# Optimization experiments

Measured on AMD Instinct MI355X. Metric: run time of the kernel, lower is better.

Reference implementation:

```python
import jax, jax.numpy as jnp
import numpy as np

B, N, L, E, U, G, R, D, C = 64, 50000, 8, 100000, 20000, 20000, 64, 16, 2


def setup_inputs() -> dict:
    rng = np.random.default_rng(0)
    key = jax.random.key(0)
    ks = jax.random.split(key, 10)
    # index structures (duplicate-free where the torch code assumes uniqueness)
    gene_map = jnp.asarray(rng.choice(N, G, replace=False).astype(np.int32))
    dst_unique = jnp.stack([jnp.asarray(rng.choice(N, U, replace=False).astype(np.int32)) for _ in range(L)])
    root_ids = jnp.asarray(rng.choice(N, R, replace=False).astype(np.int32))
    src = jax.random.randint(ks[0], (L, E), 0, N, dtype=jnp.int32)
    dst_pos = jax.random.randint(ks[1], (L, E), 0, U, dtype=jnp.int32)
    # data and parameters
    X_gene_batch = jax.random.normal(ks[2], (B, G), jnp.float32)
    w_in = jax.random.normal(ks[3], (D,), jnp.float32) * 0.5   # Linear(1, d) weight
    b_in = jax.random.normal(ks[4], (D,), jnp.float32) * 0.1
    W = jax.random.normal(ks[5], (L, D, D), jnp.float32) * (1.0 / np.sqrt(D))  # xavier-ish
    bias = jnp.zeros((N, D), jnp.float32)
    W_head = jax.random.normal(ks[6], (C, R * D), jnp.float32) * (1.0 / np.sqrt(R * D))
    b_head = jnp.zeros((C,), jnp.float32)
    return {
        "X_gene_batch": X_gene_batch, "w_in": w_in, "b_in": b_in, "W": W,
        "bias": bias, "W_head": W_head, "b_head": b_head,
        "gene_map": gene_map, "src": src, "dst_pos": dst_pos,
        "dst_unique": dst_unique, "root_ids": root_ids,
    }


def reference(X_gene_batch, w_in, b_in, W, bias, W_head, b_head,
              gene_map, src, dst_pos, dst_unique, root_ids):
    Bn = X_gene_batch.shape[0]
    n_nodes, d = bias.shape
    n_layers = W.shape[0]
    u = dst_unique.shape[1]
    # _init_state_vector: h=0, scatter in_proj(X[...,None]) at gene_map
    gene_emb = X_gene_batch[..., None] * w_in + b_in          # [B, G, d]
    h = jnp.zeros((Bn, n_nodes, d), X_gene_batch.dtype)
    h = h.at[:, gene_map].set(gene_emb)
    for li in range(n_layers):
        h_src = h[:, src[li]]                                  # gather [B, E, d]
        msg = jnp.einsum('bed,df->bef', h_src, W[li])          # small dxd matmul
        agg = jnp.zeros((Bn, u, d), h.dtype).at[:, dst_pos[li]].add(msg)  # scatter-add
        h_dst = jnp.tanh(agg + bias[dst_unique[li]][None])     # bias lookup + tanh (dropout=0)
        h = h.at[:, dst_unique[li]].set(h_dst)                 # write back
    feat = h[:, root_ids].reshape(Bn, -1)                      # roots_concat readout
    return feat @ W_head.T + b_head                            # [B, C]
```

## Files before the change

### kernel.cpp

```cpp
#include <hip/hip_runtime.h>
#include <hip/hip_fp16.h>
#include <cmath>

constexpr int B_ = 64, N_ = 50000, L_ = 8, E_ = 100000, U_ = 20000, G_ = 20000, R_ = 64, D_ = 16, C_ = 2;
constexpr int EPL_ = E_ + 3 * U_ + 4096;
constexpr int EPLG_ = EPL_ / 4 + 16;
constexpr int GPW = 8;
constexpr int BC = 64;
constexpr int F = BC * 2;


__device__ __forceinline__ float tanh_fast(float x) {
  float e = __expf(2.0f * x);
  return 1.0f - 2.0f * __builtin_amdgcn_rcpf(e + 1.0f);
}


__global__ __launch_bounds__(256) void hist_kernel(
    const int* __restrict__ dst_pos, int* __restrict__ cnt,
    int* __restrict__ rank) {
  int e = blockIdx.x * 256 + threadIdx.x;
  int li = blockIdx.y;
  if (e >= E_) return;
  rank[li * E_ + e] = atomicAdd(&cnt[li * U_ + dst_pos[li * E_ + e]], 1);
}

__global__ __launch_bounds__(1024) void scan_kernel(
    const int* __restrict__ cnt, int* __restrict__ offs) {
  __shared__ int sums[1024];
  int li = blockIdx.x, t = threadIdx.x;
  int base = t * 20;
  int v[20];
  int s = 0;
#pragma unroll
  for (int i = 0; i < 20; ++i) {
    int idx = base + i;
    int c = (idx < U_) ? cnt[li * U_ + idx] : -1;
    int pc = (c < 0) ? 0 : ((c == 0) ? 4 : ((c + 3) & ~3));
    v[i] = s;
    s += pc;
  }
  sums[t] = s;
  __syncthreads();
  for (int off = 1; off < 1024; off <<= 1) {
    int o = (t >= off) ? sums[t - off] : 0;
    __syncthreads();
    sums[t] += o;
    __syncthreads();
  }
  int excl = sums[t] - s;
#pragma unroll
  for (int i = 0; i < 20; ++i) {
    int idx = base + i;
    if (idx < U_) offs[li * (U_ + 1) + idx] = excl + v[i];
  }
  if (t == 1023) offs[li * (U_ + 1) + U_] = sums[1023];
}

__global__ __launch_bounds__(256) void scatter_kernel(
    const int* __restrict__ dst_pos, const int* __restrict__ src,
    const int* __restrict__ offs, const int* __restrict__ rank,
    int* __restrict__ ssrc) {
  int e = blockIdx.x * 256 + threadIdx.x;
  int li = blockIdx.y;
  if (e >= E_) return;
  int u = dst_pos[li * E_ + e];
  int p = offs[li * (U_ + 1) + u] + rank[li * E_ + e];
  ssrc[(size_t)li * EPL_ + p] = src[li * E_ + e];
}

__global__ __launch_bounds__(256) void pad_fill_ug_k(
    const int* __restrict__ cnt, const int* __restrict__ offs,
    int* __restrict__ ssrc, int* __restrict__ ug) {
  int t = blockIdx.x * 256 + threadIdx.x;
  if (t >= L_ * U_) return;
  int li = t / U_, u = t % U_;
  int start = offs[li * (U_ + 1) + u];
  int end = start + cnt[li * U_ + u];
  int pend = offs[li * (U_ + 1) + u + 1];
  int* sp = ssrc + (size_t)li * EPL_;
  for (int p = end; p < pend; ++p) sp[p] = N_;
  int* ugp = ug + (size_t)li * EPLG_;
  for (int g = start >> 2; g < (pend >> 2); ++g) ugp[g] = u;
  if (u == U_ - 1) {
    int ptot = offs[li * (U_ + 1) + U_];
    for (int p = ptot; p < ptot + 8; ++p) sp[p] = N_;
  }
}


__global__ __launch_bounds__(256) void gene_init_k(
    const float* __restrict__ X, const float* __restrict__ w_in,
    const float* __restrict__ b_in, const int* __restrict__ gene_map,
    float4* __restrict__ h4) {
  int t = blockIdx.x * 256 + threadIdx.x;
  if (t >= G_ * BC) return;
  int b = t % BC;
  int g = t / BC;
  float x = X[b * G_ + g];
  int node = gene_map[g];
  float4 out[2];
  __half2* oh = reinterpret_cast<__half2*>(out);
#pragma unroll
  for (int k = 0; k < 8; ++k) {
    float r0 = fmaf(x, w_in[2 * k], b_in[2 * k]);
    float r1 = fmaf(x, w_in[2 * k + 1], b_in[2 * k + 1]);
    oh[k] = __float22half2_rn(make_float2(r0, r1));
  }
  h4[(size_t)node * F + b * 2] = out[0];
  h4[(size_t)node * F + b * 2 + 1] = out[1];
}

__global__ __launch_bounds__(256) void gather_k(
    const float4* __restrict__ h4, const int* __restrict__ ug,
    const int* __restrict__ ssrc, float4* __restrict__ agg4, int li) {
  int tid = threadIdx.x;
  int wave = tid >> 6, lane = tid & 63;
  int wv = blockIdx.x * 4 + wave;
  int g0 = wv * GPW, gend = g0 + GPW;
  const int* ugp = ug + (size_t)li * EPLG_;
  const int* sp = ssrc + (size_t)li * EPL_;

  int prevU = (g0 == 0) ? -2 : ugp[g0 - 1];
  int g = g0;
  while (g < gend && ugp[g] == prevU) ++g;
  if (g >= gend) return;
  int curU = ugp[g];
  if (curU < 0) return;

  __half2 acc[2][2][4];
  const __half2 z = __half2half2(__float2half(0.f));
#pragma unroll
  for (int j = 0; j < 2; ++j)
#pragma unroll
    for (int r = 0; r < 2; ++r)
#pragma unroll
      for (int k = 0; k < 4; ++k) acc[j][r][k] = z;

  auto flushu = [&](int u) {
#pragma unroll
    for (int r = 0; r < 2; ++r) {
      float4 outv;
      __half2* ov = reinterpret_cast<__half2*>(&outv);
#pragma unroll
      for (int k = 0; k < 4; ++k) {
        float2 f0 = __half22float2(acc[0][r][k]);
        float2 f1 = __half22float2(acc[1][r][k]);
        ov[k] = __float22half2_rn(make_float2(f0.x + f1.x, f0.y + f1.y));
      }
      agg4[(size_t)u * F + lane + r * 64] = outv;
    }
#pragma unroll
    for (int j = 0; j < 2; ++j)
#pragma unroll
      for (int r = 0; r < 2; ++r)
#pragma unroll
        for (int k = 0; k < 4; ++k) acc[j][r][k] = z;
  };

  auto loadRows = [&](float4 (&v)[4][2], int4 id) {
    v[0][0] = h4[(size_t)id.x * F + lane]; v[0][1] = h4[(size_t)id.x * F + lane + 64];
    v[1][0] = h4[(size_t)id.y * F + lane]; v[1][1] = h4[(size_t)id.y * F + lane + 64];
    v[2][0] = h4[(size_t)id.z * F + lane]; v[2][1] = h4[(size_t)id.z * F + lane + 64];
    v[3][0] = h4[(size_t)id.w * F + lane]; v[3][1] = h4[(size_t)id.w * F + lane + 64];
  };
  auto accum = [&](const float4 (&v)[4][2]) {
#pragma unroll
    for (int j = 0; j < 4; ++j)
#pragma unroll
      for (int r = 0; r < 2; ++r) {
        const __half2* p = reinterpret_cast<const __half2*>(&v[j][r]);
#pragma unroll
        for (int k = 0; k < 4; ++k)
          acc[j & 1][r][k] = __hadd2(acc[j & 1][r][k], p[k]);
      }
  };

  float4 va[4][2], vb[4][2];
  int4 idA = *(const int4*)(sp + 4 * g);
  loadRows(va, idA);
  int nuA = ugp[g + 1];
  int nuB;

  for (;;) {
    {
      bool more = (nuA >= 0) && ((nuA == curU) || (g + 1 < gend));
      if (more) {
        int4 idB = *(const int4*)(sp + 4 * (g + 1));
        loadRows(vb, idB);
        nuB = ugp[g + 2];
      }
      accum(va);
      if (nuA != curU) {
        flushu(curU);
        if (!more) return;
        curU = nuA;
      }
      ++g;
    }
    {
      bool more = (nuB >= 0) && ((nuB == curU) || (g + 1 < gend));
      if (more) {
        int4 idA2 = *(const int4*)(sp + 4 * (g + 1));
        loadRows(va, idA2);
        nuA = ugp[g + 2];
      }
      accum(vb);
      if (nuB != curU) {
        flushu(curU);
        if (!more) return;
        curU = nuB;
      }
      ++g;
    }
  }
}

__global__ __launch_bounds__(256) void dense_k(
    const float4* __restrict__ agg4, const float* __restrict__ W,
    const float* __restrict__ bias, const int* __restrict__ dst_unique,
    float4* __restrict__ h4, int li) {
  __shared__ float Wlds[256];
  int tid = threadIdx.x;
  Wlds[tid] = W[li * 256 + tid];
  __syncthreads();
  int t = blockIdx.x * 256 + tid;
  int u = t >> 6, b = t & 63;
  float4 c0 = agg4[(size_t)u * F + b * 2];
  float4 c1 = agg4[(size_t)u * F + b * 2 + 1];
  float a[16];
  {
    const __half2* p0 = reinterpret_cast<const __half2*>(&c0);
    const __half2* p1 = reinterpret_cast<const __half2*>(&c1);
#pragma unroll
    for (int k = 0; k < 4; ++k) {
      float2 f0 = __half22float2(p0[k]);
      float2 f1 = __half22float2(p1[k]);
      a[2 * k] = f0.x; a[2 * k + 1] = f0.y;
      a[8 + 2 * k] = f1.x; a[8 + 2 * k + 1] = f1.y;
    }
  }
  float m[16];
#pragma unroll
  for (int j = 0; j < 16; ++j) m[j] = 0.f;
#pragma unroll
  for (int d = 0; d < 16; ++d) {
    float s = a[d];
    const float4* wr = (const float4*)&Wlds[d * 16];
    float4 w0 = wr[0], w1 = wr[1], w2 = wr[2], w3 = wr[3];
    m[0] = fmaf(s, w0.x, m[0]);  m[1] = fmaf(s, w0.y, m[1]);
    m[2] = fmaf(s, w0.z, m[2]);  m[3] = fmaf(s, w0.w, m[3]);
    m[4] = fmaf(s, w1.x, m[4]);  m[5] = fmaf(s, w1.y, m[5]);
    m[6] = fmaf(s, w1.z, m[6]);  m[7] = fmaf(s, w1.w, m[7]);
    m[8] = fmaf(s, w2.x, m[8]);  m[9] = fmaf(s, w2.y, m[9]);
    m[10] = fmaf(s, w2.z, m[10]); m[11] = fmaf(s, w2.w, m[11]);
    m[12] = fmaf(s, w3.x, m[12]); m[13] = fmaf(s, w3.y, m[13]);
    m[14] = fmaf(s, w3.z, m[14]); m[15] = fmaf(s, w3.w, m[15]);
  }
  int node = dst_unique[li * U_ + u];
  const float4* bp = (const float4*)(bias + (size_t)node * 16);
  float4 b0 = bp[0], b1 = bp[1], b2 = bp[2], b3 = bp[3];
  float bb[16] = {b0.x, b0.y, b0.z, b0.w, b1.x, b1.y, b1.z, b1.w,
                  b2.x, b2.y, b2.z, b2.w, b3.x, b3.y, b3.z, b3.w};
  float4 o0, o1;
  __half2* ov0 = reinterpret_cast<__half2*>(&o0);
  __half2* ov1 = reinterpret_cast<__half2*>(&o1);
#pragma unroll
  for (int k = 0; k < 4; ++k) {
    ov0[k] = __float22half2_rn(make_float2(tanh_fast(m[2 * k] + bb[2 * k]),
                                           tanh_fast(m[2 * k + 1] + bb[2 * k + 1])));
    ov1[k] = __float22half2_rn(make_float2(tanh_fast(m[8 + 2 * k] + bb[8 + 2 * k]),
                                           tanh_fast(m[8 + 2 * k + 1] + bb[8 + 2 * k + 1])));
  }
  h4[(size_t)node * F + b * 2] = o0;
  h4[(size_t)node * F + b * 2 + 1] = o1;
}

__global__ __launch_bounds__(64) void head_k(
    const float4* __restrict__ h4, const float* __restrict__ W_head,
    const float* __restrict__ b_head, const int* __restrict__ root_ids,
    float* __restrict__ out) {
  int bl = blockIdx.x;
  int r = threadIdx.x;
  int node = root_ids[r];
  float4 p0 = h4[(size_t)node * F + bl * 2];
  float4 p1 = h4[(size_t)node * F + bl * 2 + 1];
  float v[16];
  const __half2* ph0 = reinterpret_cast<const __half2*>(&p0);
  const __half2* ph1 = reinterpret_cast<const __half2*>(&p1);
#pragma unroll
  for (int k = 0; k < 4; ++k) {
    float2 f0 = __half22float2(ph0[k]);
    float2 f1 = __half22float2(ph1[k]);
    v[2 * k] = f0.x; v[2 * k + 1] = f0.y;
    v[8 + 2 * k] = f1.x; v[8 + 2 * k + 1] = f1.y;
  }
  float acc0 = 0.f, acc1 = 0.f;
#pragma unroll
  for (int d = 0; d < 16; ++d) {
    acc0 = fmaf(v[d], W_head[r * 16 + d], acc0);
    acc1 = fmaf(v[d], W_head[1024 + r * 16 + d], acc1);
  }
  for (int off = 32; off; off >>= 1) {
    acc0 += __shfl_down(acc0, off, 64);
    acc1 += __shfl_down(acc1, off, 64);
  }
  if (r == 0) {
    out[bl * 2 + 0] = acc0 + b_head[0];
    out[bl * 2 + 1] = acc1 + b_head[1];
  }
}

__global__ void zero_out_k(float* out, int n) {
  int t = blockIdx.x * 256 + threadIdx.x;
  if (t < n) out[t] = 0.f;
}


static size_t need_bytes() {
  return (size_t)(N_ + 1) * F * 16 + (size_t)U_ * F * 16 +
         (size_t)L_ * U_ * 4 +
         (size_t)L_ * (U_ + 1) * 4 +
         (size_t)L_ * E_ * 4 +
         (size_t)L_ * EPL_ * 4;
}

extern "C" void kernel_launch(void* const* d_in, const int* in_sizes, int n_in,
                              void* d_out, int out_size, void* d_ws, size_t ws_size,
                              hipStream_t stream) {
  if (ws_size < need_bytes()) {
    zero_out_k<<<(out_size + 255) / 256, 256, 0, stream>>>((float*)d_out, out_size);
    return;
  }
  const float* X = (const float*)d_in[0];
  const float* w_in = (const float*)d_in[1];
  const float* b_in = (const float*)d_in[2];
  const float* W = (const float*)d_in[3];
  const float* bias = (const float*)d_in[4];
  const float* W_head = (const float*)d_in[5];
  const float* b_head = (const float*)d_in[6];
  const int* gene_map = (const int*)d_in[7];
  const int* src = (const int*)d_in[8];
  const int* dst_pos = (const int*)d_in[9];
  const int* dst_unique = (const int*)d_in[10];
  const int* root_ids = (const int*)d_in[11];
  float* out = (float*)d_out;

  const size_t h_bytes = (size_t)(N_ + 1) * F * 16;
  const size_t agg_bytes = (size_t)U_ * F * 16;
  const size_t cnt_bytes = (size_t)L_ * U_ * 4;
  const size_t offs_bytes = (size_t)L_ * (U_ + 1) * 4;
  const size_t rank_bytes = (size_t)L_ * E_ * 4;
  const size_t ug_bytes = (size_t)L_ * EPLG_ * 4;

  char* ws = (char*)d_ws;
  float4* h4 = (float4*)ws;
  float4* agg4 = (float4*)(ws + h_bytes);
  int* cnt = (int*)(ws + h_bytes + agg_bytes);
  int* offs = (int*)(ws + h_bytes + agg_bytes + cnt_bytes);
  int* rank = (int*)(ws + h_bytes + agg_bytes + cnt_bytes + offs_bytes);
  int* ug = rank;
  int* ssrc = (int*)(ws + h_bytes + agg_bytes + cnt_bytes + offs_bytes + rank_bytes);
  (void)ug_bytes;

  hipMemsetAsync(cnt, 0, cnt_bytes, stream);
  hipMemsetAsync(h4, 0, h_bytes, stream);
  dim3 egrid((E_ + 255) / 256, L_);
  hist_kernel<<<egrid, 256, 0, stream>>>(dst_pos, cnt, rank);
  scan_kernel<<<L_, 1024, 0, stream>>>(cnt, offs);
  scatter_kernel<<<egrid, 256, 0, stream>>>(dst_pos, src, offs, rank, ssrc);
  hipMemsetAsync(ug, 0xFF, ug_bytes, stream);
  pad_fill_ug_k<<<(L_ * U_ + 255) / 256, 256, 0, stream>>>(cnt, offs, ssrc, ug);

  gene_init_k<<<(G_ * BC + 255) / 256, 256, 0, stream>>>(X, w_in, b_in, gene_map, h4);

  const int total_groups = EPL_ / 4;
  const int gwaves = (total_groups + GPW - 1) / GPW;
  const int gather_grid = (gwaves + 3) / 4;
  const int dense_grid = U_ * BC / 256;
  for (int li = 0; li < L_; ++li) {
    gather_k<<<gather_grid, 256, 0, stream>>>(h4, ug, ssrc, agg4, li);
    dense_k<<<dense_grid, 256, 0, stream>>>(agg4, W, bias, dst_unique, h4, li);
  }

  head_k<<<BC, 64, 0, stream>>>(h4, W_head, b_head, root_ids, out);
}
```

Measured before the change: 631.2 us.

## Split gather rows across two waves, deepen prefetch, and fuse padding into scan

The gather kernel now assigns each group span to two waves, each handling one half of the 128-float4 row. It adds an 8-deep ring of index prefetches with 4 outstanding row-load batches, which raises memory-level parallelism per wave while lowering register use per wave. The padding and ug-fill work moves into the scan kernel, which removes one kernel launch and one memset. ug gets its own workspace region instead of aliasing rank, which is needed because rank is still being read while the scatter kernel runs. The cost is a larger workspace, duplicated index loads across the two waves, and serial per-thread fill loops inside the single-block-per-layer scan.

```diff
diff --git a/kernel.cpp b/kernel.cpp
--- a/kernel.cpp
+++ b/kernel.cpp
@@ -25,17 +25,20 @@
   rank[li * E_ + e] = atomicAdd(&cnt[li * U_ + dst_pos[li * E_ + e]], 1);
 }
 
-__global__ __launch_bounds__(1024) void scan_kernel(
-    const int* __restrict__ cnt, int* __restrict__ offs) {
+__global__ __launch_bounds__(1024) void scan_pad_kernel(
+    const int* __restrict__ cnt, int* __restrict__ offs,
+    int* __restrict__ ssrc, int* __restrict__ ug) {
   __shared__ int sums[1024];
   int li = blockIdx.x, t = threadIdx.x;
   int base = t * 20;
+  int cr[20];
   int v[20];
   int s = 0;
 #pragma unroll
   for (int i = 0; i < 20; ++i) {
     int idx = base + i;
     int c = (idx < U_) ? cnt[li * U_ + idx] : -1;
+    cr[i] = c;
     int pc = (c < 0) ? 0 : ((c == 0) ? 4 : ((c + 3) & ~3));
     v[i] = s;
     s += pc;
@@ -49,12 +52,24 @@
     __syncthreads();
   }
   int excl = sums[t] - s;
+  int* sp = ssrc + (size_t)li * EPL_;
+  int* ugp = ug + (size_t)li * EPLG_;
 #pragma unroll
   for (int i = 0; i < 20; ++i) {
     int idx = base + i;
-    if (idx < U_) offs[li * (U_ + 1) + idx] = excl + v[i];
-  }
-  if (t == 1023) offs[li * (U_ + 1) + U_] = sums[1023];
+    if (idx >= U_) break;
+    int start = excl + v[i];
+    int c = cr[i];
+    int pc = (c == 0) ? 4 : ((c + 3) & ~3);
+    int pend = start + pc;
+    offs[li * (U_ + 1) + idx] = start;
+    for (int p = start + c; p < pend; ++p) sp[p] = N_;
+    for (int gq = start >> 2; gq < (pend >> 2); ++gq) ugp[gq] = idx;
+  }
+  int ptot = sums[1023];
+  if (t == 1023) offs[li * (U_ + 1) + U_] = ptot;
+  for (int p = ptot + t; p < EPL_; p += 1024) sp[p] = N_;
+  for (int gq = (ptot >> 2) + t; gq < EPLG_; gq += 1024) ugp[gq] = -1;
 }
 
 __global__ __launch_bounds__(256) void scatter_kernel(
@@ -67,25 +82,6 @@
   int u = dst_pos[li * E_ + e];
   int p = offs[li * (U_ + 1) + u] + rank[li * E_ + e];
   ssrc[(size_t)li * EPL_ + p] = src[li * E_ + e];
-}
-
-__global__ __launch_bounds__(256) void pad_fill_ug_k(
-    const int* __restrict__ cnt, const int* __restrict__ offs,
-    int* __restrict__ ssrc, int* __restrict__ ug) {
-  int t = blockIdx.x * 256 + threadIdx.x;
-  if (t >= L_ * U_) return;
-  int li = t / U_, u = t % U_;
-  int start = offs[li * (U_ + 1) + u];
-  int end = start + cnt[li * U_ + u];
-  int pend = offs[li * (U_ + 1) + u + 1];
-  int* sp = ssrc + (size_t)li * EPL_;
-  for (int p = end; p < pend; ++p) sp[p] = N_;
-  int* ugp = ug + (size_t)li * EPLG_;
-  for (int g = start >> 2; g < (pend >> 2); ++g) ugp[g] = u;
-  if (u == U_ - 1) {
-    int ptot = offs[li * (U_ + 1) + U_];
-    for (int p = ptot; p < ptot + 8; ++p) sp[p] = N_;
-  }
 }
 
 
@@ -114,12 +110,16 @@
 __global__ __launch_bounds__(256) void gather_k(
     const float4* __restrict__ h4, const int* __restrict__ ug,
     const int* __restrict__ ssrc, float4* __restrict__ agg4, int li) {
+  constexpr int GCAP = EPL_ / 4;
   int tid = threadIdx.x;
-  int wave = tid >> 6, lane = tid & 63;
-  int wv = blockIdx.x * 4 + wave;
-  int g0 = wv * GPW, gend = g0 + GPW;
+  int lane = tid & 63;
+  int wv = __builtin_amdgcn_readfirstlane(blockIdx.x * 4 + (tid >> 6));
+  int span = wv >> 1, half = wv & 1;
+  int g0 = span * GPW, gend = g0 + GPW;
   const int* ugp = ug + (size_t)li * EPLG_;
   const int* sp = ssrc + (size_t)li * EPL_;
+  const float4* hb = h4 + ((half << 6) + lane);
+  float4* ab = agg4 + ((half << 6) + lane);
 
   int prevU = (g0 == 0) ? -2 : ugp[g0 - 1];
   int g = g0;
@@ -128,92 +128,103 @@
   int curU = ugp[g];
   if (curU < 0) return;
 
-  __half2 acc[2][2][4];
+  __half2 acc0[4], acc1[4];
   const __half2 z = __half2half2(__float2half(0.f));
 #pragma unroll
-  for (int j = 0; j < 2; ++j)
-#pragma unroll
-    for (int r = 0; r < 2; ++r)
-#pragma unroll
-      for (int k = 0; k < 4; ++k) acc[j][r][k] = z;
-
-  auto flushu = [&](int u) {
-#pragma unroll
-    for (int r = 0; r < 2; ++r) {
-      float4 outv;
-      __half2* ov = reinterpret_cast<__half2*>(&outv);
-#pragma unroll
-      for (int k = 0; k < 4; ++k) {
-        float2 f0 = __half22float2(acc[0][r][k]);
-        float2 f1 = __half22float2(acc[1][r][k]);
-        ov[k] = __float22half2_rn(make_float2(f0.x + f1.x, f0.y + f1.y));
-      }
-      agg4[(size_t)u * F + lane + r * 64] = outv;
+  for (int k = 0; k < 4; ++k) { acc0[k] = z; acc1[k] = z; }
+
+  auto FLUSH = [&](int u) {
+    float4 outv;
+    __half2* ov = reinterpret_cast<__half2*>(&outv);
+#pragma unroll
+    for (int k = 0; k < 4; ++k) {
+      float2 f0 = __half22float2(acc0[k]);
+      float2 f1 = __half22float2(acc1[k]);
+      ov[k] = __float22half2_rn(make_float2(f0.x + f1.x, f0.y + f1.y));
+      acc0[k] = z;
+      acc1[k] = z;
     }
-#pragma unroll
-    for (int j = 0; j < 2; ++j)
-#pragma unroll
-      for (int r = 0; r < 2; ++r)
-#pragma unroll
-        for (int k = 0; k < 4; ++k) acc[j][r][k] = z;
+    ab[(size_t)u << 7] = outv;
   };
 
-  auto loadRows = [&](float4 (&v)[4][2], int4 id) {
-    v[0][0] = h4[(size_t)id.x * F + lane]; v[0][1] = h4[(size_t)id.x * F + lane + 64];
-    v[1][0] = h4[(size_t)id.y * F + lane]; v[1][1] = h4[(size_t)id.y * F + lane + 64];
-    v[2][0] = h4[(size_t)id.z * F + lane]; v[2][1] = h4[(size_t)id.z * F + lane + 64];
-    v[3][0] = h4[(size_t)id.w * F + lane]; v[3][1] = h4[(size_t)id.w * F + lane + 64];
+  auto LDROWS = [&](float4 (&vv)[4], const int4& id) {
+    vv[0] = hb[(size_t)id.x << 7];
+    vv[1] = hb[(size_t)id.y << 7];
+    vv[2] = hb[(size_t)id.z << 7];
+    vv[3] = hb[(size_t)id.w << 7];
   };
-  auto accum = [&](const float4 (&v)[4][2]) {
-#pragma unroll
-    for (int j = 0; j < 4; ++j)
-#pragma unroll
-      for (int r = 0; r < 2; ++r) {
-        const __half2* p = reinterpret_cast<const __half2*>(&v[j][r]);
-#pragma unroll
-        for (int k = 0; k < 4; ++k)
-          acc[j & 1][r][k] = __hadd2(acc[j & 1][r][k], p[k]);
-      }
+
+  auto ACCUM = [&](const float4 (&vv)[4]) {
+    const __half2* q0 = reinterpret_cast<const __half2*>(&vv[0]);
+    const __half2* q1 = reinterpret_cast<const __half2*>(&vv[1]);
+    const __half2* q2 = reinterpret_cast<const __half2*>(&vv[2]);
+    const __half2* q3 = reinterpret_cast<const __half2*>(&vv[3]);
+#pragma unroll
+    for (int k = 0; k < 4; ++k) {
+      acc0[k] = __hadd2(acc0[k], q0[k]);
+      acc1[k] = __hadd2(acc1[k], q1[k]);
+      acc0[k] = __hadd2(acc0[k], q2[k]);
+      acc1[k] = __hadd2(acc1[k], q3[k]);
+    }
   };
 
-  float4 va[4][2], vb[4][2];
-  int4 idA = *(const int4*)(sp + 4 * g);
-  loadRows(va, idA);
-  int nuA = ugp[g + 1];
-  int nuB;
+  int gstart = g;
+  int gA = gstart & ~7;
+  int4 idq0, idq1, idq2, idq3, idq4, idq5, idq6, idq7;
+  int nu0, nu1, nu2, nu3, nu4, nu5, nu6, nu7;
+
+#define QINIT(K)                                     \
+  {                                                  \
+    int gq_ = gA + K;                                \
+    if (gq_ < gstart) {                              \
+      idq##K = make_int4(N_, N_, N_, N_);            \
+      nu##K = curU;                                  \
+    } else {                                         \
+      gq_ = (gq_ < GCAP) ? gq_ : GCAP - 1;           \
+      idq##K = *(const int4*)(sp + 4 * gq_);         \
+      nu##K = ugp[gq_ + 1];                          \
+    }                                                \
+  }
+  QINIT(0) QINIT(1) QINIT(2) QINIT(3) QINIT(4) QINIT(5) QINIT(6) QINIT(7)
+
+  float4 v0[4], v1[4], v2[4], v3[4];
+  LDROWS(v0, idq0);
+  LDROWS(v1, idq1);
+  LDROWS(v2, idq2);
+  LDROWS(v3, idq3);
+  g = gA;
+
+#define PHASE(K, VB, IDU)                            \
+  {                                                  \
+    ACCUM(VB);                                       \
+    int nu_ = nu##K;                                 \
+    if (nu_ != curU) {                               \
+      FLUSH(curU);                                   \
+      if (nu_ < 0 || g + 1 >= gend) return;          \
+      curU = nu_;                                    \
+    }                                                \
+    ++g;                                             \
+    {                                                \
+      int gq_ = g + 7;                               \
+      gq_ = (gq_ < GCAP) ? gq_ : GCAP - 1;           \
+      idq##K = *(const int4*)(sp + 4 * gq_);         \
+      nu##K = ugp[gq_ + 1];                          \
+    }                                                \
+    LDROWS(VB, idq##IDU);                            \
+  }
 
   for (;;) {
-    {
-      bool more = (nuA >= 0) && ((nuA == curU) || (g + 1 < gend));
-      if (more) {
-        int4 idB = *(const int4*)(sp + 4 * (g + 1));
-        loadRows(vb, idB);
-        nuB = ugp[g + 2];
-      }
-      accum(va);
-      if (nuA != curU) {
-        flushu(curU);
-        if (!more) return;
-        curU = nuA;
-      }
-      ++g;
-    }
-    {
-      bool more = (nuB >= 0) && ((nuB == curU) || (g + 1 < gend));
-      if (more) {
-        int4 idA2 = *(const int4*)(sp + 4 * (g + 1));
-        loadRows(va, idA2);
-        nuA = ugp[g + 2];
-      }
-      accum(vb);
-      if (nuB != curU) {
-        flushu(curU);
-        if (!more) return;
-        curU = nuB;
-      }
-      ++g;
-    }
-  }
+    PHASE(0, v0, 4)
+    PHASE(1, v1, 5)
+    PHASE(2, v2, 6)
+    PHASE(3, v3, 7)
+    PHASE(4, v0, 0)
+    PHASE(5, v1, 1)
+    PHASE(6, v2, 2)
+    PHASE(7, v3, 3)
+  }
+#undef PHASE
+#undef QINIT
 }
 
 __global__ __launch_bounds__(256) void dense_k(
@@ -224,8 +235,8 @@
   int tid = threadIdx.x;
   Wlds[tid] = W[li * 256 + tid];
   __syncthreads();
-  int t = blockIdx.x * 256 + tid;
-  int u = t >> 6, b = t & 63;
+  int u = __builtin_amdgcn_readfirstlane(blockIdx.x * 4 + (tid >> 6));
+  int b = tid & 63;
   float4 c0 = agg4[(size_t)u * F + b * 2];
   float4 c1 = agg4[(size_t)u * F + b * 2 + 1];
   float a[16];
@@ -322,7 +333,8 @@
          (size_t)L_ * U_ * 4 +
          (size_t)L_ * (U_ + 1) * 4 +
          (size_t)L_ * E_ * 4 +
-         (size_t)L_ * EPL_ * 4;
+         (size_t)L_ * EPL_ * 4 +
+         (size_t)L_ * EPLG_ * 4;
 }
 
 extern "C" void kernel_launch(void* const* d_in, const int* in_sizes, int n_in,
@@ -351,7 +363,7 @@
   const size_t cnt_bytes = (size_t)L_ * U_ * 4;
   const size_t offs_bytes = (size_t)L_ * (U_ + 1) * 4;
   const size_t rank_bytes = (size_t)L_ * E_ * 4;
-  const size_t ug_bytes = (size_t)L_ * EPLG_ * 4;
+  const size_t ssrc_bytes = (size_t)L_ * EPL_ * 4;
 
   char* ws = (char*)d_ws;
   float4* h4 = (float4*)ws;
@@ -359,24 +371,22 @@
   int* cnt = (int*)(ws + h_bytes + agg_bytes);
   int* offs = (int*)(ws + h_bytes + agg_bytes + cnt_bytes);
   int* rank = (int*)(ws + h_bytes + agg_bytes + cnt_bytes + offs_bytes);
-  int* ug = rank;
   int* ssrc = (int*)(ws + h_bytes + agg_bytes + cnt_bytes + offs_bytes + rank_bytes);
-  (void)ug_bytes;
+  int* ug = (int*)(ws + h_bytes + agg_bytes + cnt_bytes + offs_bytes + rank_bytes + ssrc_bytes);
 
   hipMemsetAsync(cnt, 0, cnt_bytes, stream);
   hipMemsetAsync(h4, 0, h_bytes, stream);
   dim3 egrid((E_ + 255) / 256, L_);
   hist_kernel<<<egrid, 256, 0, stream>>>(dst_pos, cnt, rank);
-  scan_kernel<<<L_, 1024, 0, stream>>>(cnt, offs);
+  scan_pad_kernel<<<L_, 1024, 0, stream>>>(cnt, offs, ssrc, ug);
   scatter_kernel<<<egrid, 256, 0, stream>>>(dst_pos, src, offs, rank, ssrc);
-  hipMemsetAsync(ug, 0xFF, ug_bytes, stream);
-  pad_fill_ug_k<<<(L_ * U_ + 255) / 256, 256, 0, stream>>>(cnt, offs, ssrc, ug);
 
   gene_init_k<<<(G_ * BC + 255) / 256, 256, 0, stream>>>(X, w_in, b_in, gene_map, h4);
 
   const int total_groups = EPL_ / 4;
   const int gwaves = (total_groups + GPW - 1) / GPW;
-  const int gather_grid = (gwaves + 3) / 4;
+  const int gather_waves = gwaves * 2;
+  const int gather_grid = (gather_waves + 3) / 4;
   const int dense_grid = U_ * BC / 256;
   for (int li = 0; li < L_; ++li) {
     gather_k<<<gather_grid, 256, 0, stream>>>(h4, ug, ssrc, agg4, li);
```

After: 716.7 us. 13.5% more time.

## Fuse padding into scan and deepen gather prefetch to three stages

Applied to the files above, without the earlier changes.

Merges the pad-fill and ug-labeling pass into the scan kernel, which removes one kernel launch and one memset. ug gets its own workspace region instead of aliasing rank. The gather kernel moves from a 2-deep to a 3-deep software pipeline of row loads, computes its stop group up front, and uses readfirstlane to keep wave indices scalar. This hides more gather latency at the cost of extra registers, and the scan kernel now does serial padding writes per thread.

```diff
diff --git a/kernel.cpp b/kernel.cpp
--- a/kernel.cpp
+++ b/kernel.cpp
@@ -25,17 +25,20 @@
   rank[li * E_ + e] = atomicAdd(&cnt[li * U_ + dst_pos[li * E_ + e]], 1);
 }
 
-__global__ __launch_bounds__(1024) void scan_kernel(
-    const int* __restrict__ cnt, int* __restrict__ offs) {
+__global__ __launch_bounds__(1024) void scan_pad_kernel(
+    const int* __restrict__ cnt, int* __restrict__ offs,
+    int* __restrict__ ssrc, int* __restrict__ ug) {
   __shared__ int sums[1024];
   int li = blockIdx.x, t = threadIdx.x;
   int base = t * 20;
+  int cr[20];
   int v[20];
   int s = 0;
 #pragma unroll
   for (int i = 0; i < 20; ++i) {
     int idx = base + i;
     int c = (idx < U_) ? cnt[li * U_ + idx] : -1;
+    cr[i] = c;
     int pc = (c < 0) ? 0 : ((c == 0) ? 4 : ((c + 3) & ~3));
     v[i] = s;
     s += pc;
@@ -49,12 +52,24 @@
     __syncthreads();
   }
   int excl = sums[t] - s;
+  int* sp = ssrc + (size_t)li * EPL_;
+  int* ugp = ug + (size_t)li * EPLG_;
 #pragma unroll
   for (int i = 0; i < 20; ++i) {
     int idx = base + i;
-    if (idx < U_) offs[li * (U_ + 1) + idx] = excl + v[i];
-  }
-  if (t == 1023) offs[li * (U_ + 1) + U_] = sums[1023];
+    if (idx >= U_) break;
+    int start = excl + v[i];
+    int c = cr[i];
+    int pc = (c == 0) ? 4 : ((c + 3) & ~3);
+    int pend = start + pc;
+    offs[li * (U_ + 1) + idx] = start;
+    for (int p = start + c; p < pend; ++p) sp[p] = N_;
+    for (int gq = start >> 2; gq < (pend >> 2); ++gq) ugp[gq] = idx;
+  }
+  int ptot = sums[1023];
+  if (t == 1023) offs[li * (U_ + 1) + U_] = ptot;
+  for (int p = ptot + t; p < EPL_; p += 1024) sp[p] = N_;
+  for (int gq = (ptot >> 2) + t; gq < EPLG_; gq += 1024) ugp[gq] = -1;
 }
 
 __global__ __launch_bounds__(256) void scatter_kernel(
@@ -67,25 +82,6 @@
   int u = dst_pos[li * E_ + e];
   int p = offs[li * (U_ + 1) + u] + rank[li * E_ + e];
   ssrc[(size_t)li * EPL_ + p] = src[li * E_ + e];
-}
-
-__global__ __launch_bounds__(256) void pad_fill_ug_k(
-    const int* __restrict__ cnt, const int* __restrict__ offs,
-    int* __restrict__ ssrc, int* __restrict__ ug) {
-  int t = blockIdx.x * 256 + threadIdx.x;
-  if (t >= L_ * U_) return;
-  int li = t / U_, u = t % U_;
-  int start = offs[li * (U_ + 1) + u];
-  int end = start + cnt[li * U_ + u];
-  int pend = offs[li * (U_ + 1) + u + 1];
-  int* sp = ssrc + (size_t)li * EPL_;
-  for (int p = end; p < pend; ++p) sp[p] = N_;
-  int* ugp = ug + (size_t)li * EPLG_;
-  for (int g = start >> 2; g < (pend >> 2); ++g) ugp[g] = u;
-  if (u == U_ - 1) {
-    int ptot = offs[li * (U_ + 1) + U_];
-    for (int p = ptot; p < ptot + 8; ++p) sp[p] = N_;
-  }
 }
 
 
@@ -114,9 +110,10 @@
 __global__ __launch_bounds__(256) void gather_k(
     const float4* __restrict__ h4, const int* __restrict__ ug,
     const int* __restrict__ ssrc, float4* __restrict__ agg4, int li) {
+  constexpr int GCAP = EPL_ / 4;
   int tid = threadIdx.x;
-  int wave = tid >> 6, lane = tid & 63;
-  int wv = blockIdx.x * 4 + wave;
+  int lane = tid & 63;
+  int wv = __builtin_amdgcn_readfirstlane(blockIdx.x * 4 + (tid >> 6));
   int g0 = wv * GPW, gend = g0 + GPW;
   const int* ugp = ug + (size_t)li * EPLG_;
   const int* sp = ssrc + (size_t)li * EPL_;
@@ -127,6 +124,16 @@
   if (g >= gend) return;
   int curU = ugp[g];
   if (curU < 0) return;
+
+  int uend = ugp[gend - 1];
+  int gstop;
+  if (uend < 0) {
+    gstop = g;
+    while (ugp[gstop] >= 0) ++gstop;
+  } else {
+    gstop = gend;
+    while (ugp[gstop] == uend) ++gstop;
+  }
 
   __half2 acc[2][2][4];
   const __half2 z = __half2half2(__float2half(0.f));
@@ -176,44 +183,42 @@
       }
   };
 
-  float4 va[4][2], vb[4][2];
-  int4 idA = *(const int4*)(sp + 4 * g);
-  loadRows(va, idA);
+  auto CLG = [&](int q) { return (q < GCAP) ? q : GCAP - 1; };
+
+  int4 id0 = *(const int4*)(sp + 4 * g);
+  int4 id1 = *(const int4*)(sp + 4 * CLG(g + 1));
+  int4 idP = *(const int4*)(sp + 4 * CLG(g + 2));
+  int4 idQ = *(const int4*)(sp + 4 * CLG(g + 3));
+  int4 idR;
   int nuA = ugp[g + 1];
-  int nuB;
+  int nuB = ugp[CLG(g + 1) + 1];
+  int nuC = ugp[CLG(g + 2) + 1];
+
+  float4 va[4][2], vb[4][2], vc[4][2];
+  loadRows(va, id0);
+  loadRows(vb, id1);
+
+#define PHASE(VACC, VLD, IDLD, IDPF, NUCUR)          \
+  {                                                  \
+    loadRows(VLD, IDLD);                             \
+    IDPF = *(const int4*)(sp + 4 * CLG(g + 4));      \
+    int nuCur = NUCUR;                               \
+    NUCUR = ugp[CLG(g + 3) + 1];                     \
+    accum(VACC);                                     \
+    if (nuCur != curU) {                             \
+      flushu(curU);                                  \
+      if (g + 1 >= gstop) return;                    \
+      curU = nuCur;                                  \
+    }                                                \
+    ++g;                                             \
+  }
 
   for (;;) {
-    {
-      bool more = (nuA >= 0) && ((nuA == curU) || (g + 1 < gend));
-      if (more) {
-        int4 idB = *(const int4*)(sp + 4 * (g + 1));
-        loadRows(vb, idB);
-        nuB = ugp[g + 2];
-      }
-      accum(va);
-      if (nuA != curU) {
-        flushu(curU);
-        if (!more) return;
-        curU = nuA;
-      }
-      ++g;
-    }
-    {
-      bool more = (nuB >= 0) && ((nuB == curU) || (g + 1 < gend));
-      if (more) {
-        int4 idA2 = *(const int4*)(sp + 4 * (g + 1));
-        loadRows(va, idA2);
-        nuA = ugp[g + 2];
-      }
-      accum(vb);
-      if (nuB != curU) {
-        flushu(curU);
-        if (!more) return;
-        curU = nuB;
-      }
-      ++g;
-    }
-  }
+    PHASE(va, vc, idP, idR, nuA)
+    PHASE(vb, va, idQ, idP, nuB)
+    PHASE(vc, vb, idR, idQ, nuC)
+  }
+#undef PHASE
 }
 
 __global__ __launch_bounds__(256) void dense_k(
@@ -224,8 +229,8 @@
   int tid = threadIdx.x;
   Wlds[tid] = W[li * 256 + tid];
   __syncthreads();
-  int t = blockIdx.x * 256 + tid;
-  int u = t >> 6, b = t & 63;
+  int u = __builtin_amdgcn_readfirstlane(blockIdx.x * 4 + (tid >> 6));
+  int b = tid & 63;
   float4 c0 = agg4[(size_t)u * F + b * 2];
   float4 c1 = agg4[(size_t)u * F + b * 2 + 1];
   float a[16];
@@ -322,7 +327,8 @@
          (size_t)L_ * U_ * 4 +
          (size_t)L_ * (U_ + 1) * 4 +
          (size_t)L_ * E_ * 4 +
-         (size_t)L_ * EPL_ * 4;
+         (size_t)L_ * EPL_ * 4 +
+         (size_t)L_ * EPLG_ * 4;
 }
 
 extern "C" void kernel_launch(void* const* d_in, const int* in_sizes, int n_in,
@@ -351,7 +357,7 @@
   const size_t cnt_bytes = (size_t)L_ * U_ * 4;
   const size_t offs_bytes = (size_t)L_ * (U_ + 1) * 4;
   const size_t rank_bytes = (size_t)L_ * E_ * 4;
-  const size_t ug_bytes = (size_t)L_ * EPLG_ * 4;
+  const size_t ssrc_bytes = (size_t)L_ * EPL_ * 4;
 
   char* ws = (char*)d_ws;
   float4* h4 = (float4*)ws;
@@ -359,18 +365,15 @@
   int* cnt = (int*)(ws + h_bytes + agg_bytes);
   int* offs = (int*)(ws + h_bytes + agg_bytes + cnt_bytes);
   int* rank = (int*)(ws + h_bytes + agg_bytes + cnt_bytes + offs_bytes);
-  int* ug = rank;
   int* ssrc = (int*)(ws + h_bytes + agg_bytes + cnt_bytes + offs_bytes + rank_bytes);
-  (void)ug_bytes;
+  int* ug = (int*)(ws + h_bytes + agg_bytes + cnt_bytes + offs_bytes + rank_bytes + ssrc_bytes);
 
   hipMemsetAsync(cnt, 0, cnt_bytes, stream);
   hipMemsetAsync(h4, 0, h_bytes, stream);
   dim3 egrid((E_ + 255) / 256, L_);
   hist_kernel<<<egrid, 256, 0, stream>>>(dst_pos, cnt, rank);
-  scan_kernel<<<L_, 1024, 0, stream>>>(cnt, offs);
+  scan_pad_kernel<<<L_, 1024, 0, stream>>>(cnt, offs, ssrc, ug);
   scatter_kernel<<<egrid, 256, 0, stream>>>(dst_pos, src, offs, rank, ssrc);
-  hipMemsetAsync(ug, 0xFF, ug_bytes, stream);
-  pad_fill_ug_k<<<(L_ * U_ + 255) / 256, 256, 0, stream>>>(cnt, offs, ssrc, ug);
 
   gene_init_k<<<(G_ * BC + 255) / 256, 256, 0, stream>>>(X, w_in, b_in, gene_map, h4);
 
```

Measured after the change: 670.5 us. 6.2% more time.
